# Performance work log

Hardware: AMD Instinct MI355X
Metric: run time of the kernel (lower is better)

## Reference

```python
import jax, jax.numpy as jnp
import numpy as np
from jax import lax

EPS = 1e-5  # BatchNorm eps (inference mode: running_mean=m, running_var=v)
DN = ('NCDHW', 'OIDHW', 'NCDHW')


def _conv_bn_relu(x, W, b, g, bt, m, v, pad):
    y = lax.conv_general_dilated(x, W, window_strides=(1, 1, 1), padding=pad,
                                 dimension_numbers=DN)
    y = y + b[None, :, None, None, None]
    scale = g / jnp.sqrt(v + EPS)
    y = (y - m[None, :, None, None, None]) * scale[None, :, None, None, None] \
        + bt[None, :, None, None, None]
    return jax.nn.relu(y)


def _cal_patt(k, q, v):
    # spatial non-local attention over H*W, independently per (n, c, d)
    N, C, D, H, W = q.shape
    qf = q.reshape(N, C, D, H * W)
    kf = k.reshape(N, C, D, H * W)
    vf = v.reshape(N, C, D, H * W)
    # sigma[n,c,d,i,j] = q_i * k_j ; softmax over j ; out[j] = sum_i v_i * r_ij
    sigma = qf[..., :, None] * kf[..., None, :]          # [N,C,D,HW,HW]
    r = jax.nn.softmax(sigma, axis=-1)
    out = jnp.einsum('ncdi,ncdij->ncdj', vf, r)
    return out.reshape(N, C, D, H, W)


def _cal_datt(k, q, v):
    # temporal non-local attention over D, independently per (n, c, h, w)
    N, C, D, H, W = q.shape
    qf = jnp.transpose(q, (0, 1, 3, 4, 2))               # [N,C,H,W,D]
    kf = jnp.transpose(k, (0, 1, 3, 4, 2))
    vf = jnp.transpose(v, (0, 1, 3, 4, 2))
    sigma = qf[..., :, None] * kf[..., None, :]          # [N,C,H,W,D,D]
    r = jax.nn.softmax(sigma, axis=-1)
    out = jnp.einsum('nchwi,nchwij->nchwj', vf, r)
    return jnp.transpose(out, (0, 1, 4, 2, 3))           # back to [N,C,D,H,W]


def setup_inputs() -> dict:
    key = jax.random.key(0)
    ks = jax.random.split(key, 8)
    C, Cc = 512, 64  # features_, features_//compress
    N, D, H, W = 2, 8, 16, 16
    f32 = jnp.float32

    def bn(c):
        return (jnp.ones((c,), f32), jnp.zeros((c,), f32),
                jnp.zeros((c,), f32), jnp.ones((c,), f32))

    x = jax.random.normal(ks[0], (N, C, D, H, W), f32)
    Wq = jax.random.normal(ks[1], (Cc, C, 1, 1, 1), f32) * 0.04
    Wk = jax.random.normal(ks[2], (Cc, C, 1, 1, 1), f32) * 0.04
    Wv = jax.random.normal(ks[3], (Cc, C, 1, 1, 1), f32) * 0.04
    Ws = jax.random.normal(ks[4], (C, Cc, 3, 3, 3), f32) * 0.02
    Wd = jax.random.normal(ks[5], (C, Cc, 3, 3, 3), f32) * 0.02
    gq, btq, mq, vq = bn(Cc)
    gk, btk, mk, vk = bn(Cc)
    gv, btv, mv, vv = bn(Cc)
    gs, bts, ms, vs = bn(C)
    gd, btd, md, vd = bn(C)
    return dict(
        x=x, gama=jnp.float32(0.5),
        Wq=Wq, bq=jnp.zeros((Cc,), f32), gq=gq, btq=btq, mq=mq, vq=vq,
        Wk=Wk, bk=jnp.zeros((Cc,), f32), gk=gk, btk=btk, mk=mk, vk=vk,
        Wv=Wv, bv=jnp.zeros((Cc,), f32), gv=gv, btv=btv, mv=mv, vv=vv,
        Ws=Ws, bs=jnp.zeros((C,), f32), gs=gs, bts=bts, ms=ms, vs=vs,
        Wd=Wd, bd=jnp.zeros((C,), f32), gd=gd, btd=btd, md=md, vd=vd,
    )


def reference(x, gama,
              Wq, bq, gq, btq, mq, vq,
              Wk, bk, gk, btk, mk, vk,
              Wv, bv, gv, btv, mv, vv,
              Ws, bs, gs, bts, ms, vs,
              Wd, bd, gd, btd, md, vd):
    P0 = [(0, 0)] * 3
    P1 = [(1, 1)] * 3
    v_x = _conv_bn_relu(x, Wv, bv, gv, btv, mv, vv, P0)
    k_x = _conv_bn_relu(x, Wk, bk, gk, btk, mk, vk, P0)
    q_x = _conv_bn_relu(x, Wq, bq, gq, btq, mq, vq, P0)
    # name == 'st': both spatial and temporal attention branches
    Patt = _cal_patt(k_x, q_x, v_x)
    Patt_c = _conv_bn_relu(Patt, Ws, bs, gs, bts, ms, vs, P1)
    Datt = _cal_datt(k_x, q_x, v_x)
    Datt_c = _conv_bn_relu(Datt, Wd, bd, gd, btd, md, vd, P1)
    return gama * (Datt_c + Patt_c) + x
```

## Files before the change

kernel.cpp:

```cpp
#include <hip/hip_runtime.h>
#include <cmath>

#define EPSBN 1e-5f

namespace {
constexpr int C_IN = 512;
constexpr int CC   = 64;
constexpr int CD   = 8;
constexpr int HW   = 256;
constexpr int DHW  = CD * HW;
constexpr int QSZ  = 2 * CC * DHW;

constexpr int PG    = 18 * 18;
constexpr int GPLN  = PG * 8;
constexpr int PADSZ = 2 * 10 * 8 * GPLN;
constexpr int WTSZ  = 27 * 512 * 64;

typedef __attribute__((ext_vector_type(8))) short bf16x8;
typedef __attribute__((ext_vector_type(4))) float f32x4;
typedef __attribute__((ext_vector_type(16))) float f32x16;

typedef unsigned int u32_g __attribute__((address_space(1)));
typedef unsigned int u32_l __attribute__((address_space(3)));

__device__ inline unsigned short f2bf(float f) {
    unsigned u = __float_as_uint(f);
    return (unsigned short)((u + 0x7fffu + ((u >> 16) & 1u)) >> 16);
}
}

__global__ __launch_bounds__(256) void prep_kernel(
    const float* __restrict__ Ws, const float* __restrict__ Wd,
    const float* __restrict__ Wq, const float* __restrict__ Wk,
    const float* __restrict__ Wv,
    const float* __restrict__ bs, const float* __restrict__ gs,
    const float* __restrict__ bts, const float* __restrict__ ms,
    const float* __restrict__ vs,
    const float* __restrict__ bd, const float* __restrict__ gd,
    const float* __restrict__ btd, const float* __restrict__ md,
    const float* __restrict__ vd,
    uint4* __restrict__ pads, unsigned short* __restrict__ Wt,
    unsigned short* __restrict__ Wqkv, float2* __restrict__ BNc)
{
    int bid = blockIdx.x;
    int t = threadIdx.x;
    if (bid < 405) {
        pads[bid * 256 + t] = make_uint4(0, 0, 0, 0);
    } else if (bid < 1429) {
        int b2 = bid - 405;
        int b  = b2 >> 9;
        int co = b2 & 511;
        const float* W = b ? Wd : Ws;
        int cog = co >> 6, co_l = co & 63;
        int r  = co_l & 31, hi = co_l >> 5;
        unsigned short* o = Wt + (size_t)b * WTSZ;
        for (int k2 = t; k2 < 27 * 64; k2 += 256) {
            int ci  = k2 / 27;
            int tap = k2 - ci * 27;
            int kd = tap / 9, tapk = tap - kd * 9;
            int half = ci >> 5, cl = ci & 31;
            int cig = cl >> 4, ci16 = cl & 15;
            int ks = ci16 >> 3;
            float w = W[(size_t)co * 1728 + k2];
            int chunk = ((cog * 2 + half) * 3 + kd) * 2 + cig;
            int pg = (r * 2 + ks) ^ (r & 7);
            o[(size_t)chunk * 9216 + tapk * 1024 + hi * 512
              + pg * 8 + (ci16 & 7)] = f2bf(w);
        }
    } else if (bid < 1621) {
        int co = bid - 1429;
        const float* W = co < 64 ? Wq : co < 128 ? Wk : Wv;
        int c = co & 63;
        for (int ci = t; ci < 512; ci += 256)
            Wqkv[(size_t)co * 512 + ci] = f2bf(W[(size_t)c * 512 + ci]);
    } else {
        int gid = (bid - 1621) * 256 + t;
        if (gid < 1024) {
            int br = gid >> 9, co = gid & 511;
            float s, o;
            if (br == 0) {
                s = gs[co] * rsqrtf(vs[co] + EPSBN);
                o = (bs[co] - ms[co]) * s + bts[co];
            } else {
                s = gd[co] * rsqrtf(vd[co] + EPSBN);
                o = (bd[co] - md[co]) * s + btd[co];
            }
            BNc[gid] = make_float2(s, o);
        }
    }
}

__global__ __launch_bounds__(256) void qkv_gemm_kernel(
    const float* __restrict__ x, const unsigned short* __restrict__ Wqkv,
    const float* __restrict__ bq, const float* __restrict__ gq,
    const float* __restrict__ btq, const float* __restrict__ mq,
    const float* __restrict__ vq,
    const float* __restrict__ bk, const float* __restrict__ gk,
    const float* __restrict__ btk, const float* __restrict__ mk,
    const float* __restrict__ vk,
    const float* __restrict__ bv, const float* __restrict__ gv,
    const float* __restrict__ btv, const float* __restrict__ mv,
    const float* __restrict__ vv,
    float* __restrict__ outq, float* __restrict__ outk, float* __restrict__ outv)
{
    int bid = blockIdx.x;
    int n = bid >> 7, p0 = (bid & 127) * 16;

    __shared__ __align__(16) unsigned short xs[16 * 512];
    int t = threadIdx.x;

    const float* xb = x + ((size_t)n * C_IN) * DHW + p0;
#pragma unroll
    for (int pass = 0; pass < 8; ++pass) {
        int idx = pass * 256 + t;
        int ci = idx >> 2, pq = idx & 3;
        float4 v4 = *reinterpret_cast<const float4*>(xb + (size_t)ci * DHW + pq * 4);
        float arr[4] = {v4.x, v4.y, v4.z, v4.w};
#pragma unroll
        for (int u = 0; u < 4; ++u) {
            int pos = pq * 4 + u;
            int boff = pos * 1024 + ((ci * 2) ^ ((pos & 7) << 4));
            *reinterpret_cast<unsigned short*>(
                reinterpret_cast<char*>(xs) + boff) = f2bf(arr[u]);
        }
    }
    __syncthreads();

    int wid = t >> 6, lane = t & 63;
    int l15 = lane & 15, l4 = lane >> 4;
    int mh = wid * 3;
    int pos = l15;

    bf16x8 bfr[16];
    const char* xsb = reinterpret_cast<const char*>(xs) + pos * 1024;
    int swz = (pos & 7) << 4;
#pragma unroll
    for (int kk = 0; kk < 16; ++kk)
        bfr[kk] = *reinterpret_cast<const bf16x8*>(xsb + ((kk * 64 + l4 * 16) ^ swz));

    f32x4 acc[3];
#pragma unroll
    for (int i = 0; i < 3; ++i) acc[i] = (f32x4){0.f, 0.f, 0.f, 0.f};

#pragma unroll
    for (int i = 0; i < 3; ++i) {
        const unsigned short* wrow =
            Wqkv + ((size_t)(mh + i) * 16 + l15) * 512 + l4 * 8;
#pragma unroll
        for (int kk = 0; kk < 16; ++kk) {
            bf16x8 af = *reinterpret_cast<const bf16x8*>(wrow + kk * 32);
            acc[i] = __builtin_amdgcn_mfma_f32_16x16x32_bf16(af, bfr[kk], acc[i], 0, 0, 0);
        }
    }

#pragma unroll
    for (int i = 0; i < 3; ++i) {
        int mf = mh + i;
        int br = mf >> 2;
        const float* bb  = br == 0 ? bq  : br == 1 ? bk  : bv;
        const float* gg  = br == 0 ? gq  : br == 1 ? gk  : gv;
        const float* bt  = br == 0 ? btq : br == 1 ? btk : btv;
        const float* mm  = br == 0 ? mq  : br == 1 ? mk  : mv;
        const float* vvp = br == 0 ? vq  : br == 1 ? vk  : vv;
        float*       op  = br == 0 ? outq : br == 1 ? outk : outv;
        int cb = (mf & 3) * 16 + l4 * 4;
#pragma unroll
        for (int r = 0; r < 4; ++r) {
            int c = cb + r;
            float s = gg[c] * rsqrtf(vvp[c] + EPSBN);
            float val = (acc[i][r] + bb[c] - mm[c]) * s + bt[c];
            op[((size_t)(n * CC + c)) * DHW + p0 + pos] = fmaxf(val, 0.f);
        }
    }
}

__global__ __launch_bounds__(256) void att_kernel(
    const float* __restrict__ q, const float* __restrict__ k,
    const float* __restrict__ v,
    unsigned short* __restrict__ Pp, unsigned short* __restrict__ Dp)
{
    __shared__ __align__(16) float sk[256], sq[256], sw[256];
    __shared__ float red[4];
    int t = threadIdx.x;
    int bid = blockIdx.x;

    if (bid < 1024) {
        int n = bid >> 9, c = (bid >> 3) & 63, d = bid & 7;
        size_t base = (size_t)bid * HW;
        float kt = k[base + t];
        float qt = q[base + t];
        float vt = v[base + t];
        sk[t] = kt;
        sq[t] = qt;

        float m = kt;
#pragma unroll
        for (int off = 32; off >= 1; off >>= 1)
            m = fmaxf(m, __shfl_xor(m, off));
        if ((t & 63) == 0) red[t >> 6] = m;
        __syncthreads();
        float kmax = fmaxf(fmaxf(red[0], red[1]), fmaxf(red[2], red[3]));

        float qkm = qt * kmax;
        float d0 = 0.f, d1 = 0.f, d2 = 0.f, d3 = 0.f;
        const float4* sk4 = reinterpret_cast<const float4*>(sk);
#pragma unroll 8
        for (int j = 0; j < 64; ++j) {
            float4 kk = sk4[j];
            d0 += __expf(fmaf(qt, kk.x, -qkm));
            d1 += __expf(fmaf(qt, kk.y, -qkm));
            d2 += __expf(fmaf(qt, kk.z, -qkm));
            d3 += __expf(fmaf(qt, kk.w, -qkm));
        }
        float den = (d0 + d1) + (d2 + d3);
        sw[t] = vt / den;
        __syncthreads();

        float kjm = kt - kmax;
        float o0 = 0.f, o1 = 0.f, o2 = 0.f, o3 = 0.f;
        const float4* sw4 = reinterpret_cast<const float4*>(sw);
        const float4* sq4 = reinterpret_cast<const float4*>(sq);
#pragma unroll 8
        for (int i = 0; i < 64; ++i) {
            float4 ww = sw4[i];
            float4 qq = sq4[i];
            o0 += ww.x * __expf(qq.x * kjm);
            o1 += ww.y * __expf(qq.y * kjm);
            o2 += ww.z * __expf(qq.z * kjm);
            o3 += ww.w * __expf(qq.w * kjm);
        }
        float o = (o0 + o1) + (o2 + o3);

        int h = t >> 4, w = t & 15;
        size_t dst = ((((size_t)(n * 10 + d + 1) * 8 + (c >> 3)) * PG)
                      + (h + 1) * 18 + (w + 1)) * 8 + (c & 7);
        Pp[dst] = f2bf(o);
    } else {
        int g = (bid - 1024) * 256 + t;
        int nc = g >> 8, hw = g & 255;
        int n = nc >> 6, c = nc & 63;
        size_t base = (size_t)nc * DHW + hw;

        float qv[8], kv[8], vv_[8];
#pragma unroll
        for (int d = 0; d < 8; ++d) {
            qv[d]  = q[base + d * HW];
            kv[d]  = k[base + d * HW];
            vv_[d] = v[base + d * HW];
        }
        float kmax = 0.f;
#pragma unroll
        for (int d = 0; d < 8; ++d) kmax = fmaxf(kmax, kv[d]);

        float wgt[8];
#pragma unroll
        for (int i = 0; i < 8; ++i) {
            float den = 0.f, qkm = qv[i] * kmax;
#pragma unroll
            for (int j = 0; j < 8; ++j)
                den += __expf(fmaf(qv[i], kv[j], -qkm));
            wgt[i] = vv_[i] / den;
        }
        int h = hw >> 4, w = hw & 15;
#pragma unroll
        for (int j = 0; j < 8; ++j) {
            float o = 0.f, kjm = kv[j] - kmax;
#pragma unroll
            for (int i = 0; i < 8; ++i)
                o += wgt[i] * __expf(qv[i] * kjm);
            size_t dst = ((((size_t)(n * 10 + j + 1) * 8 + (c >> 3)) * PG)
                          + (h + 1) * 18 + (w + 1)) * 8 + (c & 7);
            Dp[dst] = f2bf(o);
        }
    }
}

__global__ __launch_bounds__(256, 1) void conv_fused_kernel(
    const unsigned short* __restrict__ Pp, const unsigned short* __restrict__ Dp,
    const unsigned short* __restrict__ Wt,
    const float2* __restrict__ BNc,
    const float* __restrict__ x, const float* __restrict__ gama,
    float* __restrict__ out)
{
    int bid = blockIdx.x;
    int cog = bid & 7;
    int pgb = (bid >> 3) & 1;
    int sl  = bid >> 4;
    int n = sl >> 3, d = sl & 7;

    __shared__ __align__(16) unsigned short lds_i[8 * 1536];
    __shared__ __align__(16) unsigned short lds_w[2 * 18432];

    int t = threadIdx.x;
    int wid = t >> 6, lane = t & 63;
    int ph = wid & 1, br = wid >> 1;
    int col  = lane & 31;
    int wcol = lane & 15;
    int hl   = (lane >> 4) & 1;
    int ks   = lane >> 5;
    int gA   = ((col * 2 + ks) ^ (col & 7)) * 8;

    f32x16 acc[2][2];
#pragma unroll
    for (int m = 0; m < 2; ++m)
#pragma unroll
        for (int p = 0; p < 2; ++p)
#pragma unroll
            for (int r = 0; r < 16; ++r)
                acc[m][p][r] = 0.f;

#define DMAI(c_) do {                                                         \
    const int half_ = (c_) / 6, kd_ = (((c_) % 6) >> 1), cig_ = (c_) & 1;     \
    _Pragma("unroll")                                                         \
    for (int pc = 0; pc < 4; ++pc) {                                          \
        const int br_ = pc >> 1, ks_ = pc & 1;                                \
        const unsigned short* sb = (br_ ? Dp : Pp)                            \
            + ((size_t)((n * 10 + d + kd_) * 8 + half_ * 4 + cig_ * 2 + ks_)) \
              * GPLN + pgb * 1152;                                            \
        _Pragma("unroll")                                                     \
        for (int j = 0; j < 3; ++j) {                                         \
            if (((pc * 3 + j) & 3) == wid)                                    \
                __builtin_amdgcn_global_load_lds(                             \
                    (const u32_g*)(sb + j * 512 + lane * 8),                  \
                    (u32_l*)(lds_i + (((c_) & 1) * 4 + pc) * 1536 + j * 512), \
                    16, 0, 0);                                                \
        }                                                                     \
    }                                                                         \
} while (0)

#define DMAW(c_) do {                                                         \
    const int ch_ = (((cog * 2 + ((c_) / 6)) * 3 + (((c_) % 6) >> 1)) * 2     \
                     + ((c_) & 1)) * 9216;                                    \
    _Pragma("unroll")                                                         \
    for (int j = 0; j < 9; ++j) {                                             \
        int base = j * 2048 + wid * 512;                                      \
        const unsigned short* s0 = (base < 9216)                              \
            ? (Wt + ch_ + base)                                               \
            : (Wt + WTSZ + ch_ + (base - 9216));                              \
        __builtin_amdgcn_global_load_lds(                                     \
            (const u32_g*)(s0 + lane * 8),                                    \
            (u32_l*)(lds_w + ((c_) & 1) * 18432 + base), 16, 0, 0);           \
    }                                                                         \
} while (0)

#define COMPUTE(c_) do {                                                      \
    const unsigned short* wb_ = lds_w + ((c_) & 1) * 18432 + br * 9216;       \
    const unsigned short* bp_ = lds_i + (((c_) & 1) * 4 + br * 2 + ks) * 1536;\
    _Pragma("unroll")                                                         \
    for (int tapk = 0; tapk < 9; ++tapk) {                                    \
        const int kh_ = tapk / 3, kw_ = tapk % 3;                             \
        bf16x8 a0 = *(const bf16x8*)(wb_ + tapk * 1024 + gA);                 \
        bf16x8 a1 = *(const bf16x8*)(wb_ + tapk * 1024 + 512 + gA);           \
        bf16x8 b0 = *(const bf16x8*)(bp_ + ((ph * 4 + hl + kh_) * 18          \
                                     + wcol + kw_) * 8);                      \
        bf16x8 b1 = *(const bf16x8*)(bp_ + ((ph * 4 + 2 + hl + kh_) * 18      \
                                     + wcol + kw_) * 8);                      \
        acc[0][0] = __builtin_amdgcn_mfma_f32_32x32x16_bf16(a0, b0,           \
                        acc[0][0], 0, 0, 0);                                  \
        acc[0][1] = __builtin_amdgcn_mfma_f32_32x32x16_bf16(a0, b1,           \
                        acc[0][1], 0, 0, 0);                                  \
        acc[1][0] = __builtin_amdgcn_mfma_f32_32x32x16_bf16(a1, b0,           \
                        acc[1][0], 0, 0, 0);                                  \
        acc[1][1] = __builtin_amdgcn_mfma_f32_32x32x16_bf16(a1, b1,           \
                        acc[1][1], 0, 0, 0);                                  \
    }                                                                         \
} while (0)

    DMAI(0);
    DMAW(0);
    __syncthreads();

#pragma unroll
    for (int c = 0; c < 12; ++c) {
        if (c < 11) {
            DMAW(c + 1);
            DMAI(c + 1);
        }
        COMPUTE(c);
        __syncthreads();
    }

#undef DMAI
#undef DMAW
#undef COMPUTE

    float gm = gama[0];
    float* ep = reinterpret_cast<float*>(lds_w);

    if (br == 0) {
#pragma unroll
        for (int m = 0; m < 2; ++m)
#pragma unroll
            for (int p = 0; p < 2; ++p)
#pragma unroll
                for (int r = 0; r < 16; ++r) {
                    int row = (r & 3) + 8 * (r >> 2) + 4 * ks;
                    float2 c2 = BNc[cog * 64 + m * 32 + row];
                    float v = fmaxf(acc[m][p][r] * c2.x + c2.y, 0.f);
                    ep[ph * 4096 + (m * 32 + row) * 64 + p * 32 + col] = v;
                }
    }
    __syncthreads();
    if (br == 1) {
#pragma unroll
        for (int m = 0; m < 2; ++m)
#pragma unroll
            for (int p = 0; p < 2; ++p)
#pragma unroll
                for (int r = 0; r < 16; ++r) {
                    int row = (r & 3) + 8 * (r >> 2) + 4 * ks;
                    int co = cog * 64 + m * 32 + row;
                    float2 c2 = BNc[512 + co];
                    float rd = fmaxf(acc[m][p][r] * c2.x + c2.y, 0.f);
                    float rp = ep[ph * 4096 + (m * 32 + row) * 64 + p * 32 + col];
                    int pos = pgb * 128 + ph * 64 + p * 32 + col;
                    size_t oi = ((size_t)(n * 512 + co)) * 2048 + d * 256 + pos;
                    out[oi] = gm * (rp + rd) + x[oi];
                }
    }
}

extern "C" void kernel_launch(void* const* d_in, const int* in_sizes, int n_in,
                              void* d_out, int out_size, void* d_ws, size_t ws_size,
                              hipStream_t stream)
{
    const float* x    = (const float*)d_in[0];
    const float* gama = (const float*)d_in[1];
    const float* Wq  = (const float*)d_in[2];
    const float* bq  = (const float*)d_in[3];
    const float* gq  = (const float*)d_in[4];
    const float* btq = (const float*)d_in[5];
    const float* mq  = (const float*)d_in[6];
    const float* vq  = (const float*)d_in[7];
    const float* Wk  = (const float*)d_in[8];
    const float* bk  = (const float*)d_in[9];
    const float* gk  = (const float*)d_in[10];
    const float* btk = (const float*)d_in[11];
    const float* mk  = (const float*)d_in[12];
    const float* vk  = (const float*)d_in[13];
    const float* Wv  = (const float*)d_in[14];
    const float* bv  = (const float*)d_in[15];
    const float* gv  = (const float*)d_in[16];
    const float* btv = (const float*)d_in[17];
    const float* mv  = (const float*)d_in[18];
    const float* vv  = (const float*)d_in[19];
    const float* Ws  = (const float*)d_in[20];
    const float* bs  = (const float*)d_in[21];
    const float* gs  = (const float*)d_in[22];
    const float* bts = (const float*)d_in[23];
    const float* ms  = (const float*)d_in[24];
    const float* vs  = (const float*)d_in[25];
    const float* Wd  = (const float*)d_in[26];
    const float* bd  = (const float*)d_in[27];
    const float* gd  = (const float*)d_in[28];
    const float* btd = (const float*)d_in[29];
    const float* md  = (const float*)d_in[30];
    const float* vd  = (const float*)d_in[31];

    char* ws = (char*)d_ws;
    unsigned short* Pp   = (unsigned short*)ws;
    unsigned short* Dp   = Pp + PADSZ;
    unsigned short* Wt   = Dp + PADSZ;
    unsigned short* Wqkv = Wt + 2 * WTSZ;
    float* q = (float*)(ws + 5394432);
    float* k = q + QSZ;
    float* v = k + QSZ;
    float2* BNc = (float2*)(ws + 5394432 + 3 * 1048576);

    prep_kernel<<<1625, 256, 0, stream>>>(
        Ws, Wd, Wq, Wk, Wv,
        bs, gs, bts, ms, vs,
        bd, gd, btd, md, vd,
        (uint4*)Pp, Wt, Wqkv, BNc);

    qkv_gemm_kernel<<<256, 256, 0, stream>>>(
        x, Wqkv,
        bq, gq, btq, mq, vq,
        bk, gk, btk, mk, vk,
        bv, gv, btv, mv, vv,
        q, k, v);

    att_kernel<<<1152, 256, 0, stream>>>(q, k, v, Pp, Dp);

    conv_fused_kernel<<<256, 256, 0, stream>>>(
        Pp, Dp, Wt, BNc,
        x, gama, (float*)d_out);
}
```

Baseline: 67.56 us.

## Overlap next-chunk DMA with compute using partial vmcnt waits in conv pipeline

Result: no change. 66.75 us (-1.2%).

```diff
diff --git a/kernel.cpp b/kernel.cpp
--- a/kernel.cpp
+++ b/kernel.cpp
@@ -179,8 +179,7 @@
     const float* __restrict__ v,
     unsigned short* __restrict__ Pp, unsigned short* __restrict__ Dp)
 {
-    __shared__ __align__(16) float sk[256], sq[256], sw[256];
-    __shared__ float red[4];
+    __shared__ float sk[256], sq[256], sw[256], red[4];
     int t = threadIdx.x;
     int bid = blockIdx.x;
 
@@ -203,14 +202,11 @@
 
         float qkm = qt * kmax;
         float d0 = 0.f, d1 = 0.f, d2 = 0.f, d3 = 0.f;
-        const float4* sk4 = reinterpret_cast<const float4*>(sk);
-#pragma unroll 8
-        for (int j = 0; j < 64; ++j) {
-            float4 kk = sk4[j];
-            d0 += __expf(fmaf(qt, kk.x, -qkm));
-            d1 += __expf(fmaf(qt, kk.y, -qkm));
-            d2 += __expf(fmaf(qt, kk.z, -qkm));
-            d3 += __expf(fmaf(qt, kk.w, -qkm));
+        for (int j = 0; j < 256; j += 4) {
+            d0 += __expf(fmaf(qt, sk[j + 0], -qkm));
+            d1 += __expf(fmaf(qt, sk[j + 1], -qkm));
+            d2 += __expf(fmaf(qt, sk[j + 2], -qkm));
+            d3 += __expf(fmaf(qt, sk[j + 3], -qkm));
         }
         float den = (d0 + d1) + (d2 + d3);
         sw[t] = vt / den;
@@ -218,16 +214,11 @@
 
         float kjm = kt - kmax;
         float o0 = 0.f, o1 = 0.f, o2 = 0.f, o3 = 0.f;
-        const float4* sw4 = reinterpret_cast<const float4*>(sw);
-        const float4* sq4 = reinterpret_cast<const float4*>(sq);
-#pragma unroll 8
-        for (int i = 0; i < 64; ++i) {
-            float4 ww = sw4[i];
-            float4 qq = sq4[i];
-            o0 += ww.x * __expf(qq.x * kjm);
-            o1 += ww.y * __expf(qq.y * kjm);
-            o2 += ww.z * __expf(qq.z * kjm);
-            o3 += ww.w * __expf(qq.w * kjm);
+        for (int i = 0; i < 256; i += 4) {
+            o0 += sw[i + 0] * __expf(sq[i + 0] * kjm);
+            o1 += sw[i + 1] * __expf(sq[i + 1] * kjm);
+            o2 += sw[i + 2] * __expf(sq[i + 2] * kjm);
+            o3 += sw[i + 3] * __expf(sq[i + 3] * kjm);
         }
         float o = (o0 + o1) + (o2 + o3);
 
@@ -368,16 +359,21 @@
 
     DMAI(0);
     DMAW(0);
-    __syncthreads();
 
 #pragma unroll
     for (int c = 0; c < 12; ++c) {
+        if (c > 0)
+            __builtin_amdgcn_s_barrier();
         if (c < 11) {
             DMAW(c + 1);
             DMAI(c + 1);
-        }
+            asm volatile("s_waitcnt vmcnt(12)" ::: "memory");
+        } else {
+            asm volatile("s_waitcnt vmcnt(0)" ::: "memory");
+        }
+        __builtin_amdgcn_s_barrier();
+        __builtin_amdgcn_sched_barrier(0);
         COMPUTE(c);
-        __syncthreads();
     }
 
 #undef DMAI
```
